# Performance work log

Measured on AMD Instinct MI355X. Metric: run time of the kernel, lower is better.

## Reference

```python
import jax, jax.numpy as jnp
import numpy as np

B, S, D, H = 2, 2048, 1024, 16
HD = D // H  # head_dim = 64

def setup_inputs() -> dict:
    key = jax.random.key(0)
    ks = jax.random.split(key, 11)
    s = 1.0 / np.sqrt(D)
    return {
        "query_input": jax.random.normal(ks[0], (B, S, D), jnp.float32),
        "key_input":   jax.random.normal(ks[1], (B, S, D), jnp.float32),
        "value_input": jax.random.normal(ks[2], (B, S, D), jnp.float32),
        "Wq": jax.random.normal(ks[3], (D, D), jnp.float32) * s,
        "bq": jnp.zeros((D,), jnp.float32),
        "Wk": jax.random.normal(ks[4], (D, D), jnp.float32) * s,
        "bk": jnp.zeros((D,), jnp.float32),
        "Wv": jax.random.normal(ks[5], (D, D), jnp.float32) * s,
        "bv": jnp.zeros((D,), jnp.float32),
        "Wo": jax.random.normal(ks[6], (D, D), jnp.float32) * s,
        "bo": jnp.zeros((D,), jnp.float32),
    }

def _split_heads(x):
    b, s, _ = x.shape
    return x.reshape(b, s, H, HD).transpose(0, 2, 1, 3)  # [B,H,S,HD]

def reference(query_input, key_input, value_input, Wq, bq, Wk, bk, Wv, bv, Wo, bo):
    q = _split_heads(query_input @ Wq + bq)
    k = _split_heads(key_input @ Wk + bk)
    v = _split_heads(value_input @ Wv + bv)
    scores = jnp.einsum('bhqd,bhkd->bhqk', q, k) / jnp.sqrt(jnp.float32(HD))
    attn = jax.nn.softmax(scores, axis=-1)
    out = jnp.einsum('bhqk,bhkd->bhqd', attn, v)
    out = out.transpose(0, 2, 1, 3).reshape(query_input.shape[0], -1, H * HD)
    return out @ Wo + bo
```

## Files before the change

kernel.cpp:

```cpp
#include <hip/hip_runtime.h>
#include <hip/hip_bf16.h>
#include <math.h>

#define B_  2
#define S_  2048
#define D_  1024
#define H_  16
#define HD_ 64

typedef __bf16  bf16x8  __attribute__((ext_vector_type(8)));
typedef float   floatx4 __attribute__((ext_vector_type(4)));

#define MFMA16(a, b, c) __builtin_amdgcn_mfma_f32_16x16x32_bf16((a), (b), (c), 0, 0, 0)

__device__ __forceinline__ void load_lds16(const void* g, void* l) {
    __builtin_amdgcn_global_load_lds(
        (const __attribute__((address_space(1))) unsigned int*)g,
        (__attribute__((address_space(3))) unsigned int*)l, 16, 0, 0);
}

__global__ __launch_bounds__(256) void cast3_bf16_k(
    const float* __restrict__ x0, const float* __restrict__ x1, const float* __restrict__ x2,
    __hip_bfloat16* __restrict__ o0, __hip_bfloat16* __restrict__ o1, __hip_bfloat16* __restrict__ o2)
{
    const int z = blockIdx.y;
    const float* src = (z == 0) ? x0 : (z == 1) ? x1 : x2;
    __hip_bfloat16* dst = (z == 0) ? o0 : (z == 1) ? o1 : o2;
    const int i = blockIdx.x * 256 + threadIdx.x;
    const float4* s4 = (const float4*)src;
    const float4 a = s4[2 * i + 0];
    const float4 b = s4[2 * i + 1];
    union { __hip_bfloat16 h[8]; uint4 v; } p;
    p.h[0] = __float2bfloat16(a.x); p.h[1] = __float2bfloat16(a.y);
    p.h[2] = __float2bfloat16(a.z); p.h[3] = __float2bfloat16(a.w);
    p.h[4] = __float2bfloat16(b.x); p.h[5] = __float2bfloat16(b.y);
    p.h[6] = __float2bfloat16(b.z); p.h[7] = __float2bfloat16(b.w);
    ((uint4*)dst)[i] = p.v;
}

__global__ __launch_bounds__(256) void transpose4_cast_k(
    const float* __restrict__ W0, const float* __restrict__ W1,
    const float* __restrict__ W2, const float* __restrict__ W3,
    __hip_bfloat16* __restrict__ T0, __hip_bfloat16* __restrict__ T1,
    __hip_bfloat16* __restrict__ T2, __hip_bfloat16* __restrict__ T3)
{
    const int z = blockIdx.z;
    const float* W = (z == 0) ? W0 : (z == 1) ? W1 : (z == 2) ? W2 : W3;
    __hip_bfloat16* Wt = (z == 0) ? T0 : (z == 1) ? T1 : (z == 2) ? T2 : T3;

    __shared__ float T[64][65];
    const int t  = threadIdx.x;
    const int n0 = blockIdx.x * 64, k0 = blockIdx.y * 64;
    #pragma unroll
    for (int i = 0; i < 4; ++i) {
        const int u = t + i * 256;
        const int r = u >> 4, c4 = (u & 15) * 4;
        const float4 v = *(const float4*)(W + (size_t)(k0 + r) * D_ + n0 + c4);
        T[r][c4 + 0] = v.x; T[r][c4 + 1] = v.y; T[r][c4 + 2] = v.z; T[r][c4 + 3] = v.w;
    }
    __syncthreads();
    #pragma unroll
    for (int i = 0; i < 4; ++i) {
        const int u = t + i * 256;
        const int n = u >> 4, c4 = (u & 15) * 4;
        union { __hip_bfloat16 h[4]; uint2 v; } p;
        #pragma unroll
        for (int j = 0; j < 4; ++j) p.h[j] = __float2bfloat16(T[c4 + j][n]);
        *(uint2*)(Wt + (size_t)(n0 + n) * D_ + k0 + c4) = p.v;
    }
}

__global__ __launch_bounds__(256) void gemm_qkv_k(
    const __hip_bfloat16* __restrict__ xq, const __hip_bfloat16* __restrict__ xk,
    const __hip_bfloat16* __restrict__ xv,
    const __hip_bfloat16* __restrict__ WqT, const __hip_bfloat16* __restrict__ WkT,
    const __hip_bfloat16* __restrict__ WvT,
    const float* __restrict__ bq, const float* __restrict__ bk, const float* __restrict__ bv,
    __hip_bfloat16* __restrict__ Qh, __hip_bfloat16* __restrict__ Kh,
    __hip_bfloat16* __restrict__ Vt)
{
    constexpr int K = 1024;
    __shared__ __align__(16) short As0[4][128][8], As1[4][128][8];
    __shared__ __align__(16) short Bs0[4][128][8], Bs1[4][128][8];

    const int z = blockIdx.z;
    const __hip_bfloat16* A  = (z == 0) ? xq  : (z == 1) ? xk  : xv;
    const __hip_bfloat16* Bt = (z == 0) ? WqT : (z == 1) ? WkT : WvT;
    const float* bias        = (z == 0) ? bq  : (z == 1) ? bk  : bv;

    const int t    = threadIdx.x;
    const int lane = t & 63, w = t >> 6;
    const int quad = lane >> 4, l16 = lane & 15;
    const int m0   = blockIdx.x * 128, n0 = blockIdx.y * 128;
    const int wm   = (w >> 1) * 64,    wn = (w & 1) * 64;

    floatx4 acc[4][4] = {};

    auto stage = [&](int k0, short (*As)[128][8], short (*Bs)[128][8]) {
        #pragma unroll
        for (int i = 0; i < 2; ++i) {
            const int c = t + i * 256;
            const int kq = c >> 7, m = c & 127;
            load_lds16(A + (size_t)(m0 + m) * K + k0 + kq * 8, &As[kq][m][0]);
        }
        #pragma unroll
        for (int i = 0; i < 2; ++i) {
            const int c = t + i * 256;
            const int kq = c >> 7, n = c & 127;
            load_lds16(Bt + (size_t)(n0 + n) * K + k0 + kq * 8, &Bs[kq][n][0]);
        }
    };

    auto compute = [&](short (*As)[128][8], short (*Bs)[128][8]) {
        bf16x8 af[4], bfr[4];
        #pragma unroll
        for (int mt = 0; mt < 4; ++mt) af[mt]  = *(const bf16x8*)&As[quad][wm + mt * 16 + l16][0];
        #pragma unroll
        for (int nt = 0; nt < 4; ++nt) bfr[nt] = *(const bf16x8*)&Bs[quad][wn + nt * 16 + l16][0];
        #pragma unroll
        for (int mt = 0; mt < 4; ++mt)
            #pragma unroll
            for (int nt = 0; nt < 4; ++nt)
                acc[mt][nt] = MFMA16(af[mt], bfr[nt], acc[mt][nt]);
    };

    stage(0, As0, Bs0);
    for (int k0 = 0; k0 < K; k0 += 64) {
        __syncthreads();
        stage(k0 + 32, As1, Bs1);
        compute(As0, Bs0);
        __syncthreads();
        if (k0 + 64 < K) stage(k0 + 64, As0, Bs0);
        compute(As1, Bs1);
    }

    const float oscale = (z == 0) ? 0.125f : 1.0f;
    __hip_bfloat16* outp = (z == 0) ? Qh : (z == 1) ? Kh : Vt;

    #pragma unroll
    for (int mt = 0; mt < 4; ++mt)
        #pragma unroll
        for (int nt = 0; nt < 4; ++nt) {
            const int gn = n0 + wn + nt * 16 + l16;
            const float bi = bias[gn];
            #pragma unroll
            for (int r = 0; r < 4; ++r) {
                const int gm = m0 + wm + mt * 16 + quad * 4 + r;
                const float v = (acc[mt][nt][r] + bi) * oscale;
                if (z != 2) {
                    outp[(((size_t)(gm >> 11) * H_ + (gn >> 6)) * S_ + (gm & 2047)) * 64 + (gn & 63)] =
                        __float2bfloat16(v);
                } else {
                    outp[(((size_t)(gm >> 11) * H_ + (gn >> 6)) * 64 + (gn & 63)) * S_ + (gm & 2047)] =
                        __float2bfloat16(v);
                }
            }
        }
}

__global__ __launch_bounds__(256) void gemm_oproj_k(
    const __hip_bfloat16* __restrict__ A, const __hip_bfloat16* __restrict__ Bt,
    const float* __restrict__ bias, float* __restrict__ out)
{
    constexpr int K = 1024, N = 1024;
    __shared__ __align__(16) short As0[4][128][8], As1[4][128][8];
    __shared__ __align__(16) short Bs0[4][64][8],  Bs1[4][64][8];

    const int t    = threadIdx.x;
    const int lane = t & 63, w = t >> 6;
    const int quad = lane >> 4, l16 = lane & 15;
    const int m0   = blockIdx.x * 128, n0 = blockIdx.y * 64;
    const int wm   = (w >> 1) * 64,    wn = (w & 1) * 32;

    floatx4 acc[4][2] = {};

    auto stage = [&](int k0, short (*As)[128][8], short (*Bs)[64][8]) {
        #pragma unroll
        for (int i = 0; i < 2; ++i) {
            const int c = t + i * 256;
            const int kq = c >> 7, m = c & 127;
            load_lds16(A + (size_t)(m0 + m) * K + k0 + kq * 8, &As[kq][m][0]);
        }
        {
            const int kq = t >> 6, n = t & 63;
            load_lds16(Bt + (size_t)(n0 + n) * K + k0 + kq * 8, &Bs[kq][n][0]);
        }
    };

    auto compute = [&](short (*As)[128][8], short (*Bs)[64][8]) {
        bf16x8 af[4], bfr[2];
        #pragma unroll
        for (int mt = 0; mt < 4; ++mt) af[mt]  = *(const bf16x8*)&As[quad][wm + mt * 16 + l16][0];
        #pragma unroll
        for (int nt = 0; nt < 2; ++nt) bfr[nt] = *(const bf16x8*)&Bs[quad][wn + nt * 16 + l16][0];
        #pragma unroll
        for (int mt = 0; mt < 4; ++mt)
            #pragma unroll
            for (int nt = 0; nt < 2; ++nt)
                acc[mt][nt] = MFMA16(af[mt], bfr[nt], acc[mt][nt]);
    };

    stage(0, As0, Bs0);
    for (int k0 = 0; k0 < K; k0 += 64) {
        __syncthreads();
        stage(k0 + 32, As1, Bs1);
        compute(As0, Bs0);
        __syncthreads();
        if (k0 + 64 < K) stage(k0 + 64, As0, Bs0);
        compute(As1, Bs1);
    }

    #pragma unroll
    for (int mt = 0; mt < 4; ++mt)
        #pragma unroll
        for (int nt = 0; nt < 2; ++nt) {
            const int gn = n0 + wn + nt * 16 + l16;
            const float bi = bias[gn];
            #pragma unroll
            for (int r = 0; r < 4; ++r) {
                const int gm = m0 + wm + mt * 16 + quad * 4 + r;
                out[(size_t)gm * N + gn] = acc[mt][nt][r] + bi;
            }
        }
}

__global__ __launch_bounds__(512) void attn_mfma_k(
    const __hip_bfloat16* __restrict__ Qh, const __hip_bfloat16* __restrict__ Kh,
    const __hip_bfloat16* __restrict__ Vt, __hip_bfloat16* __restrict__ Ctx)
{
    __shared__ __align__(16) short Ks0[8][64][8], Ks1[8][64][8];
    __shared__ __align__(16) short Vs0[8][64][8], Vs1[8][64][8];
    __shared__ __align__(16) __hip_bfloat16 Ps[128][72];

    const int t    = threadIdx.x;
    const int lane = t & 63, w = t >> 6;
    const int quad = lane >> 4, l16 = lane & 15;
    const int b = blockIdx.z, h = blockIdx.x;
    const size_t bh = (size_t)b * H_ + h;
    const int q0 = blockIdx.y * 128;
    const int myrow = w * 16;

    bf16x8 qf[2];
    {
        const __hip_bfloat16* qb = Qh + (bh * S_ + q0 + myrow + l16) * 64;
        qf[0] = *(const bf16x8*)(qb + quad * 8);
        qf[1] = *(const bf16x8*)(qb + 32 + quad * 8);
    }

    floatx4 oacc[4] = {};
    float lsum[4] = {0.f, 0.f, 0.f, 0.f};

    auto stage = [&](int kt, short (*Ks)[64][8], short (*Vs)[64][8]) {
        const int kq = t >> 6, p = t & 63;
        load_lds16(Kh + (bh * S_ + kt * 64 + p) * 64 + kq * 8, &Ks[kq][p][0]);
        load_lds16(Vt + (bh * 64 + p) * S_ + kt * 64 + kq * 8, &Vs[kq][p][0]);
    };

    auto compute = [&](short (*Ks)[64][8], short (*Vs)[64][8]) {
        floatx4 sacc[4] = {};
        #pragma unroll
        for (int ks = 0; ks < 2; ++ks)
            #pragma unroll
            for (int nt = 0; nt < 4; ++nt) {
                const bf16x8 kf = *(const bf16x8*)&Ks[ks * 4 + quad][nt * 16 + l16][0];
                sacc[nt] = MFMA16(qf[ks], kf, sacc[nt]);
            }
        #pragma unroll
        for (int nt = 0; nt < 4; ++nt)
            #pragma unroll
            for (int r = 0; r < 4; ++r) {
                const float p = __expf(sacc[nt][r]);
                lsum[r] += p;
                Ps[myrow + quad * 4 + r][nt * 16 + l16] = __float2bfloat16(p);
            }
        #pragma unroll
        for (int ks = 0; ks < 2; ++ks) {
            const bf16x8 pf = *(const bf16x8*)&Ps[myrow + l16][ks * 32 + quad * 8];
            #pragma unroll
            for (int nt = 0; nt < 4; ++nt) {
                const bf16x8 vf = *(const bf16x8*)&Vs[ks * 4 + quad][nt * 16 + l16][0];
                oacc[nt] = MFMA16(pf, vf, oacc[nt]);
            }
        }
    };

    stage(0, Ks0, Vs0);
    for (int kt = 0; kt < S_ / 64; kt += 2) {
        __syncthreads();
        stage(kt + 1, Ks1, Vs1);
        compute(Ks0, Vs0);
        __syncthreads();
        if (kt + 2 < S_ / 64) stage(kt + 2, Ks0, Vs0);
        compute(Ks1, Vs1);
    }

    #pragma unroll
    for (int off = 1; off < 16; off <<= 1)
        #pragma unroll
        for (int r = 0; r < 4; ++r) lsum[r] += __shfl_xor(lsum[r], off, 64);

    #pragma unroll
    for (int nt = 0; nt < 4; ++nt)
        #pragma unroll
        for (int r = 0; r < 4; ++r) {
            const int qrow = q0 + myrow + quad * 4 + r;
            Ctx[((size_t)b * S_ + qrow) * D_ + h * 64 + nt * 16 + l16] =
                __float2bfloat16(oacc[nt][r] / lsum[r]);
        }
}

extern "C" void kernel_launch(void* const* d_in, const int* in_sizes, int n_in,
                              void* d_out, int out_size, void* d_ws, size_t ws_size,
                              hipStream_t stream)
{
    const float* xq = (const float*)d_in[0];
    const float* xk = (const float*)d_in[1];
    const float* xv = (const float*)d_in[2];
    const float* Wq = (const float*)d_in[3];
    const float* bq = (const float*)d_in[4];
    const float* Wk = (const float*)d_in[5];
    const float* bk = (const float*)d_in[6];
    const float* Wv = (const float*)d_in[7];
    const float* bv = (const float*)d_in[8];
    const float* Wo = (const float*)d_in[9];
    const float* bo = (const float*)d_in[10];
    float* out = (float*)d_out;

    const size_t n = (size_t)B_ * S_ * D_;
    char* p = (char*)d_ws;
    __hip_bfloat16* xqb = (__hip_bfloat16*)p;            p += n * 2;
    __hip_bfloat16* xkb = (__hip_bfloat16*)p;            p += n * 2;
    __hip_bfloat16* xvb = (__hip_bfloat16*)p;            p += n * 2;
    __hip_bfloat16* WqT = (__hip_bfloat16*)p;            p += (size_t)D_ * D_ * 2;
    __hip_bfloat16* WkT = (__hip_bfloat16*)p;            p += (size_t)D_ * D_ * 2;
    __hip_bfloat16* WvT = (__hip_bfloat16*)p;            p += (size_t)D_ * D_ * 2;
    __hip_bfloat16* WoT = (__hip_bfloat16*)p;            p += (size_t)D_ * D_ * 2;
    __hip_bfloat16* Qh  = (__hip_bfloat16*)p;            p += n * 2;
    __hip_bfloat16* Kh  = (__hip_bfloat16*)p;            p += n * 2;
    __hip_bfloat16* Vth = (__hip_bfloat16*)p;            p += n * 2;
    __hip_bfloat16* Ctx = (__hip_bfloat16*)p;            p += n * 2;

    cast3_bf16_k<<<dim3((int)(n / 8 / 256), 3), dim3(256), 0, stream>>>(
        xq, xk, xv, xqb, xkb, xvb);
    transpose4_cast_k<<<dim3(16, 16, 4), dim3(256), 0, stream>>>(
        Wq, Wk, Wv, Wo, WqT, WkT, WvT, WoT);

    gemm_qkv_k<<<dim3((B_ * S_) / 128, D_ / 128, 3), dim3(256), 0, stream>>>(
        xqb, xkb, xvb, WqT, WkT, WvT, bq, bk, bv, Qh, Kh, Vth);

    attn_mfma_k<<<dim3(H_, S_ / 128, B_), dim3(512), 0, stream>>>(Qh, Kh, Vth, Ctx);

    gemm_oproj_k<<<dim3((B_ * S_) / 128, D_ / 64), dim3(256), 0, stream>>>(
        Ctx, WoT, bo, out);
}
```

Baseline: 253.4 us.

## Load GEMM operands directly from global into registers, bypassing LDS staging

Both the QKV projection and output projection GEMMs drop the LDS double-buffered staging and the per-step barriers. Each wave instead loads its MFMA fragments straight from global memory into registers, with a software double buffer in registers. This removes LDS traffic and __syncthreads, but operand reuse across waves now depends on L1/L2 caching. Each A and B tile is fetched by two waves instead of once per block, and the 16-byte loads are strided by row, so global load efficiency may drop.

```diff
diff --git a/kernel.cpp b/kernel.cpp
--- a/kernel.cpp
+++ b/kernel.cpp
@@ -80,9 +80,6 @@
     __hip_bfloat16* __restrict__ Vt)
 {
     constexpr int K = 1024;
-    __shared__ __align__(16) short As0[4][128][8], As1[4][128][8];
-    __shared__ __align__(16) short Bs0[4][128][8], Bs1[4][128][8];
-
     const int z = blockIdx.z;
     const __hip_bfloat16* A  = (z == 0) ? xq  : (z == 1) ? xk  : xv;
     const __hip_bfloat16* Bt = (z == 0) ? WqT : (z == 1) ? WkT : WvT;
@@ -94,45 +91,39 @@
     const int m0   = blockIdx.x * 128, n0 = blockIdx.y * 128;
     const int wm   = (w >> 1) * 64,    wn = (w & 1) * 64;
 
+    const __hip_bfloat16* Ab = A  + (size_t)(m0 + wm + l16) * K + quad * 8;
+    const __hip_bfloat16* Bb = Bt + (size_t)(n0 + wn + l16) * K + quad * 8;
+
     floatx4 acc[4][4] = {};
-
-    auto stage = [&](int k0, short (*As)[128][8], short (*Bs)[128][8]) {
-        #pragma unroll
-        for (int i = 0; i < 2; ++i) {
-            const int c = t + i * 256;
-            const int kq = c >> 7, m = c & 127;
-            load_lds16(A + (size_t)(m0 + m) * K + k0 + kq * 8, &As[kq][m][0]);
-        }
-        #pragma unroll
-        for (int i = 0; i < 2; ++i) {
-            const int c = t + i * 256;
-            const int kq = c >> 7, n = c & 127;
-            load_lds16(Bt + (size_t)(n0 + n) * K + k0 + kq * 8, &Bs[kq][n][0]);
-        }
-    };
-
-    auto compute = [&](short (*As)[128][8], short (*Bs)[128][8]) {
-        bf16x8 af[4], bfr[4];
-        #pragma unroll
-        for (int mt = 0; mt < 4; ++mt) af[mt]  = *(const bf16x8*)&As[quad][wm + mt * 16 + l16][0];
-        #pragma unroll
-        for (int nt = 0; nt < 4; ++nt) bfr[nt] = *(const bf16x8*)&Bs[quad][wn + nt * 16 + l16][0];
-        #pragma unroll
-        for (int mt = 0; mt < 4; ++mt)
-            #pragma unroll
-            for (int nt = 0; nt < 4; ++nt)
-                acc[mt][nt] = MFMA16(af[mt], bfr[nt], acc[mt][nt]);
-    };
-
-    stage(0, As0, Bs0);
+    bf16x8 a0[4], b0[4], a1[4], b1[4];
+
+#define QKV_LOAD(as, bs, kk)                                                     \
+    {                                                                            \
+        _Pragma("unroll")                                                        \
+        for (int mt = 0; mt < 4; ++mt)                                           \
+            as[mt] = *(const bf16x8*)(Ab + (size_t)mt * 16 * K + (kk));          \
+        _Pragma("unroll")                                                        \
+        for (int nt = 0; nt < 4; ++nt)                                           \
+            bs[nt] = *(const bf16x8*)(Bb + (size_t)nt * 16 * K + (kk));          \
+    }
+#define QKV_MFMA(as, bs)                                                         \
+    {                                                                            \
+        _Pragma("unroll")                                                        \
+        for (int mt = 0; mt < 4; ++mt)                                           \
+            _Pragma("unroll")                                                    \
+            for (int nt = 0; nt < 4; ++nt)                                       \
+                acc[mt][nt] = MFMA16(as[mt], bs[nt], acc[mt][nt]);               \
+    }
+
+    QKV_LOAD(a0, b0, 0);
     for (int k0 = 0; k0 < K; k0 += 64) {
-        __syncthreads();
-        stage(k0 + 32, As1, Bs1);
-        compute(As0, Bs0);
-        __syncthreads();
-        if (k0 + 64 < K) stage(k0 + 64, As0, Bs0);
-        compute(As1, Bs1);
-    }
+        QKV_LOAD(a1, b1, k0 + 32);
+        QKV_MFMA(a0, b0);
+        if (k0 + 64 < K) QKV_LOAD(a0, b0, k0 + 64);
+        QKV_MFMA(a1, b1);
+    }
+#undef QKV_LOAD
+#undef QKV_MFMA
 
     const float oscale = (z == 0) ? 0.125f : 1.0f;
     __hip_bfloat16* outp = (z == 0) ? Qh : (z == 1) ? Kh : Vt;
@@ -163,52 +154,45 @@
     const float* __restrict__ bias, float* __restrict__ out)
 {
     constexpr int K = 1024, N = 1024;
-    __shared__ __align__(16) short As0[4][128][8], As1[4][128][8];
-    __shared__ __align__(16) short Bs0[4][64][8],  Bs1[4][64][8];
-
     const int t    = threadIdx.x;
     const int lane = t & 63, w = t >> 6;
     const int quad = lane >> 4, l16 = lane & 15;
     const int m0   = blockIdx.x * 128, n0 = blockIdx.y * 64;
     const int wm   = (w >> 1) * 64,    wn = (w & 1) * 32;
 
+    const __hip_bfloat16* Ab = A  + (size_t)(m0 + wm + l16) * K + quad * 8;
+    const __hip_bfloat16* Bb = Bt + (size_t)(n0 + wn + l16) * K + quad * 8;
+
     floatx4 acc[4][2] = {};
-
-    auto stage = [&](int k0, short (*As)[128][8], short (*Bs)[64][8]) {
-        #pragma unroll
-        for (int i = 0; i < 2; ++i) {
-            const int c = t + i * 256;
-            const int kq = c >> 7, m = c & 127;
-            load_lds16(A + (size_t)(m0 + m) * K + k0 + kq * 8, &As[kq][m][0]);
-        }
-        {
-            const int kq = t >> 6, n = t & 63;
-            load_lds16(Bt + (size_t)(n0 + n) * K + k0 + kq * 8, &Bs[kq][n][0]);
-        }
-    };
-
-    auto compute = [&](short (*As)[128][8], short (*Bs)[64][8]) {
-        bf16x8 af[4], bfr[2];
-        #pragma unroll
-        for (int mt = 0; mt < 4; ++mt) af[mt]  = *(const bf16x8*)&As[quad][wm + mt * 16 + l16][0];
-        #pragma unroll
-        for (int nt = 0; nt < 2; ++nt) bfr[nt] = *(const bf16x8*)&Bs[quad][wn + nt * 16 + l16][0];
-        #pragma unroll
-        for (int mt = 0; mt < 4; ++mt)
-            #pragma unroll
-            for (int nt = 0; nt < 2; ++nt)
-                acc[mt][nt] = MFMA16(af[mt], bfr[nt], acc[mt][nt]);
-    };
-
-    stage(0, As0, Bs0);
+    bf16x8 a0[4], b0[2], a1[4], b1[2];
+
+#define OP_LOAD(as, bs, kk)                                                      \
+    {                                                                            \
+        _Pragma("unroll")                                                        \
+        for (int mt = 0; mt < 4; ++mt)                                           \
+            as[mt] = *(const bf16x8*)(Ab + (size_t)mt * 16 * K + (kk));          \
+        _Pragma("unroll")                                                        \
+        for (int nt = 0; nt < 2; ++nt)                                           \
+            bs[nt] = *(const bf16x8*)(Bb + (size_t)nt * 16 * K + (kk));          \
+    }
+#define OP_MFMA(as, bs)                                                          \
+    {                                                                            \
+        _Pragma("unroll")                                                        \
+        for (int mt = 0; mt < 4; ++mt)                                           \
+            _Pragma("unroll")                                                    \
+            for (int nt = 0; nt < 2; ++nt)                                       \
+                acc[mt][nt] = MFMA16(as[mt], bs[nt], acc[mt][nt]);               \
+    }
+
+    OP_LOAD(a0, b0, 0);
     for (int k0 = 0; k0 < K; k0 += 64) {
-        __syncthreads();
-        stage(k0 + 32, As1, Bs1);
-        compute(As0, Bs0);
-        __syncthreads();
-        if (k0 + 64 < K) stage(k0 + 64, As0, Bs0);
-        compute(As1, Bs1);
-    }
+        OP_LOAD(a1, b1, k0 + 32);
+        OP_MFMA(a0, b0);
+        if (k0 + 64 < K) OP_LOAD(a0, b0, k0 + 64);
+        OP_MFMA(a1, b1);
+    }
+#undef OP_LOAD
+#undef OP_MFMA
 
     #pragma unroll
     for (int mt = 0; mt < 4; ++mt)
```

Result: slower. 310.5 us (+22.5%).

## Use 4-buffer LDS ring with prefetch depth 2 and vmcnt-based waits in GEMMs

Applied to the files above, without the earlier changes.

Replaces the double-buffered LDS pipeline in the QKV and output-projection GEMMs with a 4-slot ring buffer that keeps two K-tiles of global-to-LDS loads in flight. Waits use explicit s_waitcnt vmcnt counts plus a single raw s_barrier per iteration, replacing two __syncthreads per pair of tiles. The goal is to hide global load latency and cut barrier overhead. It doubles LDS use per block, which may lower occupancy. The raw asm barrier relies on the hand-counted vmcnt values being right to avoid races.

```diff
diff --git a/kernel.cpp b/kernel.cpp
--- a/kernel.cpp
+++ b/kernel.cpp
@@ -12,6 +12,9 @@
 typedef float   floatx4 __attribute__((ext_vector_type(4)));
 
 #define MFMA16(a, b, c) __builtin_amdgcn_mfma_f32_16x16x32_bf16((a), (b), (c), 0, 0, 0)
+
+#define VMWAIT(N) asm volatile("s_waitcnt vmcnt(" #N ")" ::: "memory")
+#define BARRIER() asm volatile("s_barrier" ::: "memory")
 
 __device__ __forceinline__ void load_lds16(const void* g, void* l) {
     __builtin_amdgcn_global_load_lds(
@@ -80,8 +83,8 @@
     __hip_bfloat16* __restrict__ Vt)
 {
     constexpr int K = 1024;
-    __shared__ __align__(16) short As0[4][128][8], As1[4][128][8];
-    __shared__ __align__(16) short Bs0[4][128][8], Bs1[4][128][8];
+    __shared__ __align__(16) short As[4][4][128][8];
+    __shared__ __align__(16) short Bs[4][4][128][8];
 
     const int z = blockIdx.z;
     const __hip_bfloat16* A  = (z == 0) ? xq  : (z == 1) ? xk  : xv;
@@ -96,27 +99,28 @@
 
     floatx4 acc[4][4] = {};
 
-    auto stage = [&](int k0, short (*As)[128][8], short (*Bs)[128][8]) {
+    auto stage = [&](int kt, int buf) {
+        const int k0 = kt * 32;
         #pragma unroll
         for (int i = 0; i < 2; ++i) {
             const int c = t + i * 256;
             const int kq = c >> 7, m = c & 127;
-            load_lds16(A + (size_t)(m0 + m) * K + k0 + kq * 8, &As[kq][m][0]);
+            load_lds16(A + (size_t)(m0 + m) * K + k0 + kq * 8, &As[buf][kq][m][0]);
         }
         #pragma unroll
         for (int i = 0; i < 2; ++i) {
             const int c = t + i * 256;
             const int kq = c >> 7, n = c & 127;
-            load_lds16(Bt + (size_t)(n0 + n) * K + k0 + kq * 8, &Bs[kq][n][0]);
-        }
-    };
-
-    auto compute = [&](short (*As)[128][8], short (*Bs)[128][8]) {
+            load_lds16(Bt + (size_t)(n0 + n) * K + k0 + kq * 8, &Bs[buf][kq][n][0]);
+        }
+    };
+
+    auto compute = [&](int buf) {
         bf16x8 af[4], bfr[4];
         #pragma unroll
-        for (int mt = 0; mt < 4; ++mt) af[mt]  = *(const bf16x8*)&As[quad][wm + mt * 16 + l16][0];
-        #pragma unroll
-        for (int nt = 0; nt < 4; ++nt) bfr[nt] = *(const bf16x8*)&Bs[quad][wn + nt * 16 + l16][0];
+        for (int mt = 0; mt < 4; ++mt) af[mt]  = *(const bf16x8*)&As[buf][quad][wm + mt * 16 + l16][0];
+        #pragma unroll
+        for (int nt = 0; nt < 4; ++nt) bfr[nt] = *(const bf16x8*)&Bs[buf][quad][wn + nt * 16 + l16][0];
         #pragma unroll
         for (int mt = 0; mt < 4; ++mt)
             #pragma unroll
@@ -124,15 +128,16 @@
                 acc[mt][nt] = MFMA16(af[mt], bfr[nt], acc[mt][nt]);
     };
 
-    stage(0, As0, Bs0);
-    for (int k0 = 0; k0 < K; k0 += 64) {
-        __syncthreads();
-        stage(k0 + 32, As1, Bs1);
-        compute(As0, Bs0);
-        __syncthreads();
-        if (k0 + 64 < K) stage(k0 + 64, As0, Bs0);
-        compute(As1, Bs1);
-    }
+    stage(0, 0);
+    stage(1, 1);
+    for (int kt = 0; kt < 30; ++kt) {
+        stage(kt + 2, (kt + 2) & 3);
+        VMWAIT(8);
+        BARRIER();
+        compute(kt & 3);
+    }
+    VMWAIT(4); BARRIER(); compute(30 & 3);
+    VMWAIT(0); BARRIER(); compute(31 & 3);
 
     const float oscale = (z == 0) ? 0.125f : 1.0f;
     __hip_bfloat16* outp = (z == 0) ? Qh : (z == 1) ? Kh : Vt;
@@ -163,8 +168,8 @@
     const float* __restrict__ bias, float* __restrict__ out)
 {
     constexpr int K = 1024, N = 1024;
-    __shared__ __align__(16) short As0[4][128][8], As1[4][128][8];
-    __shared__ __align__(16) short Bs0[4][64][8],  Bs1[4][64][8];
+    __shared__ __align__(16) short As[4][4][128][8];
+    __shared__ __align__(16) short Bs[4][4][64][8];
 
     const int t    = threadIdx.x;
     const int lane = t & 63, w = t >> 6;
@@ -174,25 +179,26 @@
 
     floatx4 acc[4][2] = {};
 
-    auto stage = [&](int k0, short (*As)[128][8], short (*Bs)[64][8]) {
+    auto stage = [&](int kt, int buf) {
+        const int k0 = kt * 32;
         #pragma unroll
         for (int i = 0; i < 2; ++i) {
             const int c = t + i * 256;
             const int kq = c >> 7, m = c & 127;
-            load_lds16(A + (size_t)(m0 + m) * K + k0 + kq * 8, &As[kq][m][0]);
+            load_lds16(A + (size_t)(m0 + m) * K + k0 + kq * 8, &As[buf][kq][m][0]);
         }
         {
             const int kq = t >> 6, n = t & 63;
-            load_lds16(Bt + (size_t)(n0 + n) * K + k0 + kq * 8, &Bs[kq][n][0]);
-        }
-    };
-
-    auto compute = [&](short (*As)[128][8], short (*Bs)[64][8]) {
+            load_lds16(Bt + (size_t)(n0 + n) * K + k0 + kq * 8, &Bs[buf][kq][n][0]);
+        }
+    };
+
+    auto compute = [&](int buf) {
         bf16x8 af[4], bfr[2];
         #pragma unroll
-        for (int mt = 0; mt < 4; ++mt) af[mt]  = *(const bf16x8*)&As[quad][wm + mt * 16 + l16][0];
-        #pragma unroll
-        for (int nt = 0; nt < 2; ++nt) bfr[nt] = *(const bf16x8*)&Bs[quad][wn + nt * 16 + l16][0];
+        for (int mt = 0; mt < 4; ++mt) af[mt]  = *(const bf16x8*)&As[buf][quad][wm + mt * 16 + l16][0];
+        #pragma unroll
+        for (int nt = 0; nt < 2; ++nt) bfr[nt] = *(const bf16x8*)&Bs[buf][quad][wn + nt * 16 + l16][0];
         #pragma unroll
         for (int mt = 0; mt < 4; ++mt)
             #pragma unroll
@@ -200,15 +206,16 @@
                 acc[mt][nt] = MFMA16(af[mt], bfr[nt], acc[mt][nt]);
     };
 
-    stage(0, As0, Bs0);
-    for (int k0 = 0; k0 < K; k0 += 64) {
-        __syncthreads();
-        stage(k0 + 32, As1, Bs1);
-        compute(As0, Bs0);
-        __syncthreads();
-        if (k0 + 64 < K) stage(k0 + 64, As0, Bs0);
-        compute(As1, Bs1);
-    }
+    stage(0, 0);
+    stage(1, 1);
+    for (int kt = 0; kt < 30; ++kt) {
+        stage(kt + 2, (kt + 2) & 3);
+        VMWAIT(6);
+        BARRIER();
+        compute(kt & 3);
+    }
+    VMWAIT(3); BARRIER(); compute(30 & 3);
+    VMWAIT(0); BARRIER(); compute(31 & 3);
 
     #pragma unroll
     for (int mt = 0; mt < 4; ++mt)
```

Measured after the change: 263.4 us. +4.0%, slower.
